# Kernel optimization log

Measured on AMD Instinct MI355X. Metric: run time of the kernel, lower is better.

The kernel has to match this reference:

```python
import jax, jax.numpy as jnp
import numpy as np

VOCAB, EMB, H1, H2, T, B = 21, 128, 64, 100, 500, 1024


def lstm(x, W_ih, W_hh, b_ih, b_hh):
    # x: [B, T, D]; torch gate order i, f, g, o
    Bx, H = x.shape[0], W_hh.shape[1]
    xproj = jnp.einsum('btd,gd->btg', x, W_ih) + b_ih  # [B, T, 4H]

    def step(carry, xt):
        h, c = carry
        gates = xt + h @ W_hh.T + b_hh
        i, f, g, o = jnp.split(gates, 4, axis=-1)
        c = jax.nn.sigmoid(f) * c + jax.nn.sigmoid(i) * jnp.tanh(g)
        h = jax.nn.sigmoid(o) * jnp.tanh(c)
        return (h, c), h

    h0 = jnp.zeros((Bx, H), x.dtype)
    _, hs = jax.lax.scan(step, (h0, h0), xproj.transpose(1, 0, 2))
    return hs.transpose(1, 0, 2)  # [B, T, H]


def setup_inputs() -> dict:
    key = jax.random.key(0)
    ks = jax.random.split(key, 12)
    s = 0.05
    x_idx = jax.random.randint(ks[0], (B, T), 0, VOCAB, dtype=jnp.int32)
    emb_table = jax.random.normal(ks[1], (VOCAB, EMB), jnp.float32) * s
    emb_table = emb_table.at[0].set(0.0)  # padding_idx=0
    d = dict(
        x_idx=x_idx,
        emb_table=emb_table,
        W_ih1=jax.random.normal(ks[2], (4 * H1, EMB), jnp.float32) * s,
        W_hh1=jax.random.normal(ks[3], (4 * H1, H1), jnp.float32) * s,
        b_ih1=jax.random.normal(ks[4], (4 * H1,), jnp.float32) * s,
        b_hh1=jax.random.normal(ks[5], (4 * H1,), jnp.float32) * s,
        W_ih2=jax.random.normal(ks[6], (4 * H2, H1), jnp.float32) * s,
        W_hh2=jax.random.normal(ks[7], (4 * H2, H2), jnp.float32) * s,
        b_ih2=jax.random.normal(ks[8], (4 * H2,), jnp.float32) * s,
        b_hh2=jax.random.normal(ks[9], (4 * H2,), jnp.float32) * s,
        fc_w=jax.random.normal(ks[10], (1, H2), jnp.float32) * s,
        fc_b=jax.random.normal(ks[11], (1,), jnp.float32) * s,
    )
    return d


def reference(x_idx, emb_table, W_ih1, W_hh1, b_ih1, b_hh1,
              W_ih2, W_hh2, b_ih2, b_hh2, fc_w, fc_b):
    # embedding with padding_idx=0 (row is zero; mask keeps grads faithful)
    x = emb_table[x_idx] * (x_idx != 0)[..., None].astype(emb_table.dtype)  # [B,T,128]
    x = lstm(x, W_ih1, W_hh1, b_ih1, b_hh1)  # [B,T,64]
    # MaxPool1d(kernel=5, stride=5) over time
    Bx, Tx, D = x.shape
    Tp = Tx // 5
    x = x[:, :Tp * 5].reshape(Bx, Tp, 5, D).max(axis=2)  # [B,T/5,64]
    x = lstm(x, W_ih2, W_hh2, b_ih2, b_hh2)  # [B,T/5,100]
    h = x[:, -1, :]
    return jax.nn.sigmoid(h @ fc_w.T + fc_b)  # [B,1]
```

## Files before the change

kernel.cpp:

```cpp
#include <hip/hip_runtime.h>

#define VOCAB 21
#define EMB 128
#define H1 64
#define H2 100
#define T1 500
#define TP 100
#define NB 1024
#define LOG2E 1.44269504f

typedef __attribute__((ext_vector_type(8))) short bf16x8;
typedef __attribute__((ext_vector_type(4))) float f32x4;

__device__ __forceinline__ unsigned short f2bf(float x){
    union { float f; unsigned u; } v; v.f = x;
    return (unsigned short)((v.u + 0x8000u) >> 16);
}
__device__ __forceinline__ void bar_lds(){
    asm volatile("s_waitcnt lgkmcnt(0)\n\ts_barrier" ::: "memory");
}
__device__ __forceinline__ void wait_lds(){
    asm volatile("s_waitcnt lgkmcnt(0)" ::: "memory");
}
__device__ __forceinline__ float ex2(float x){ return __builtin_amdgcn_exp2f(x); }
__device__ __forceinline__ float rcp(float x){ return __builtin_amdgcn_rcpf(x); }

__global__ void k_table(const float* __restrict__ Wih, const float* __restrict__ emb,
                        const float* __restrict__ bih, const float* __restrict__ bhh,
                        float* __restrict__ table){
    const int p = threadIdx.x;
    const int v = blockIdx.x;
    const int orig = (p & 3) * H1 + (p >> 2);
    float s = bih[orig] + bhh[orig];
    if (v != 0){
        const float* w = Wih + orig * EMB;
        const float* e = emb + v * EMB;
        #pragma unroll 16
        for (int d = 0; d < EMB; ++d) s += w[d]*e[d];
    }
    table[v*256 + p] = s * LOG2E;
}

__global__ __launch_bounds__(256, 1) void k_lstm1(
    const int* __restrict__ xidx, const float* __restrict__ Whh,
    const float* __restrict__ tbl_g, float* __restrict__ x2){
  __shared__ __align__(16) float table[VOCAB*256];
  __shared__ __align__(16) unsigned short hbuf[2][16*64];
  __shared__ __align__(16) f32x4 glds[4*16*4];
  __shared__ int idxs[4*T1];

  const int tid = threadIdx.x;
  const int w = tid >> 6, l = tid & 63;
  const int b0 = blockIdx.x * 4;
  const int n = l & 15, kg = l >> 4;

  for (int i = tid; i < VOCAB*256; i += 256) table[i] = tbl_g[i];
  for (int i = tid; i < 4*T1; i += 256){
      int r = i / T1, t = i - r*T1;
      idxs[i] = xidx[(b0 + r)*T1 + t];
  }
  { unsigned short* hz = (unsigned short*)hbuf;
    for (int i = tid; i < 2048; i += 256) hz[i] = 0; }

  bf16x8 af[4][2];
  #pragma unroll
  for (int u = 0; u < 4; ++u){
      const int p = 16*(4*w + u) + n;
      const int orig = (p & 3)*H1 + (p >> 2);
      #pragma unroll
      for (int c = 0; c < 2; ++c){
          const float* src = Whh + orig*H1 + c*32 + kg*8;
          bf16x8 f;
          #pragma unroll
          for (int j = 0; j < 8; ++j) f[j] = (short)f2bf(src[j] * LOG2E);
          af[u][c] = f;
      }
  }

  char* hb = (char*)hbuf;
  char* gb = (char*)glds + 1024*w;
  const int swz = (n & 7) << 4;
  const int rb0 = (n*128 + 16*kg) ^ swz;
  const int rb1 = (n*128 + 64 + 16*kg) ^ swz;
  const int cell = 16*w + (l >> 2);
  const int r_c  = l & 3;
  const int wbh  = (r_c*128 + 2*cell) ^ (r_c << 4);
  const float twoL = 2.0f * LOG2E;

  float cc = 0.f, pm = -1e30f;
  __syncthreads();

  int vnext = idxs[r_c*T1];
  f32x4 tvq = *(const f32x4*)&table[vnext*256 + 4*cell];
  vnext = idxs[r_c*T1 + 1];
  const f32x4 z4 = {0.f, 0.f, 0.f, 0.f};

  int rp = 0, tm = 0, tp = 0;
  for (int t = 0; t < T1; ++t){
      bf16x8 bf0 = *(const bf16x8*)(hb + rp + rb0);
      bf16x8 bf1 = *(const bf16x8*)(hb + rp + rb1);
      #pragma unroll
      for (int u = 0; u < 4; ++u){
          f32x4 a = __builtin_amdgcn_mfma_f32_16x16x32_bf16(af[u][0], bf0, z4, 0,0,0);
          a        = __builtin_amdgcn_mfma_f32_16x16x32_bf16(af[u][1], bf1, a, 0,0,0);
          if (n < 4)
              *(f32x4*)(gb + 256*u + 64*kg + 16*n) = a;
      }
      wait_lds();
      f32x4 q = *(const f32x4*)(gb + 16*l);
      f32x4 tvn = *(const f32x4*)&table[vnext*256 + 4*cell];
      int vn2 = idxs[r_c*T1 + ((t + 2 < T1) ? (t + 2) : 0)];
      float gi = q[0] + tvq[0];
      float gf = q[1] + tvq[1];
      float gg = q[2] + tvq[2];
      float go = q[3] + tvq[3];
      float si = rcp(1.f + ex2(-gi));
      float sf = rcp(1.f + ex2(-gf));
      float so = rcp(1.f + ex2(-go));
      float tg = 1.f - 2.f*rcp(1.f + ex2(gg + gg));
      cc = sf*cc + si*tg;
      float th = 1.f - 2.f*rcp(1.f + ex2(twoL*cc));
      float h = so*th;
      const int wp = rp ^ 2048;
      *(unsigned short*)(hb + wp + wbh) = f2bf(h);
      pm = fmaxf(pm, h);
      if (++tm == 5){
          x2[(b0 + r_c)*(TP*H1) + tp*H1 + cell] = pm;
          pm = -1e30f; tm = 0; ++tp;
      }
      tvq = tvn; vnext = vn2;
      rp = wp;
      bar_lds();
  }
}

__global__ __launch_bounds__(512, 1) void k_lstm2(
    const float* __restrict__ x2, const float* __restrict__ Wih,
    const float* __restrict__ Whh, const float* __restrict__ bih,
    const float* __restrict__ bhh, const float* __restrict__ fcw,
    const float* __restrict__ fcb, float* __restrict__ out){
  __shared__ __align__(16) unsigned short blds[2][16*192];
  __shared__ __align__(16) f32x4 gl2[108*4];
  __shared__ float fcred[8][4];

  const int tid = threadIdx.x;
  const int w = tid >> 6, l = tid & 63;
  const int b0 = blockIdx.x * 4;
  const int n = l & 15, kg = l >> 4;
  const int tlo = (w < 2) ? 4*w : 8 + 3*(w - 2);
  const int nt  = (w < 2) ? 4 : 3;

  { unsigned* bz0 = (unsigned*)blds;
    for (int i = tid; i < 3072; i += 512) bz0[i] = 0; }
  { float* gz = (float*)gl2;
    for (int i = tid; i < 432*4; i += 512) gz[i] = 0.f; }

  bf16x8 af[4][6];
  #pragma unroll
  for (int u = 0; u < 4; ++u){
      if (u < nt){
          const int p = 16*(tlo + u) + n;
          const int cell_ = p >> 2, gate = p & 3;
          #pragma unroll
          for (int c = 0; c < 6; ++c){
              bf16x8 f;
              #pragma unroll
              for (int jj = 0; jj < 8; ++jj){
                  int k = c*32 + kg*8 + jj;
                  float vv = 0.f;
                  if (cell_ < H2){
                      if (k < 64)           vv = Wih[(gate*H2 + cell_)*H1 + k];
                      else if (k < 64 + H2) vv = Whh[(gate*H2 + cell_)*H2 + (k - 64)];
                  }
                  f[jj] = (short)f2bf(vv * LOG2E);
              }
              af[u][c] = f;
          }
      }
  }

  f32x4 bz[4];
  #pragma unroll
  for (int u = 0; u < 4; ++u){
      const int cu = 4*(tlo + u) + kg;
      f32x4 b = {0.f,0.f,0.f,0.f};
      if (u < nt && cu < H2){
          #pragma unroll
          for (int g = 0; g < 4; ++g) b[g] = (bih[g*H2 + cu] + bhh[g*H2 + cu]) * LOG2E;
      }
      bz[u] = b;
  }

  const bool act = (l >> 2) < 4*nt;
  const int cellc = 4*tlo + (l >> 2);
  const int r_c = l & 3;
  const float fwv = (act && cellc < H2) ? fcw[cellc] : 0.f;
  const float twoL = 2.0f * LOG2E;

  char* bb = (char*)blds;
  char* gb = (char*)gl2;
  const int swz = (n & 7) << 4;
  int rb[6];
  #pragma unroll
  for (int c = 0; c < 6; ++c) rb[c] = (n*384 + 64*c + 16*kg) ^ swz;
  const int wbh = (r_c*384 + 2*(64 + cellc)) ^ (r_c << 4);

  const int xr = (tid >> 5) & 3, xc = tid & 31;
  const int xwb = (xr*384 + 4*xc) ^ (xr << 4);
  if (tid >= 384){
      float2 v = *(const float2*)&x2[(b0 + xr)*(TP*H1) + 2*xc];
      unsigned pk = (unsigned)f2bf(v.x) | ((unsigned)f2bf(v.y) << 16);
      *(unsigned*)(bb + xwb) = pk;
  }
  float cc = 0.f, hv = 0.f;
  __syncthreads();

  int rp = 0;
  for (int t = 0; t < TP; ++t){
      float2 xn = {0.f, 0.f};
      if (tid >= 384 && t + 1 < TP)
          xn = *(const float2*)&x2[(b0 + xr)*(TP*H1) + (t+1)*H1 + 2*xc];
      bf16x8 bf[6];
      #pragma unroll
      for (int c = 0; c < 6; ++c) bf[c] = *(const bf16x8*)(bb + rp + rb[c]);
      #pragma unroll
      for (int u = 0; u < 4; ++u){
          if (u < nt){
              f32x4 za = __builtin_amdgcn_mfma_f32_16x16x32_bf16(af[u][0], bf[0], bz[u], 0,0,0);
              f32x4 zb = __builtin_amdgcn_mfma_f32_16x16x32_bf16(af[u][1], bf[1], (f32x4){0.f,0.f,0.f,0.f}, 0,0,0);
              za = __builtin_amdgcn_mfma_f32_16x16x32_bf16(af[u][2], bf[2], za, 0,0,0);
              zb = __builtin_amdgcn_mfma_f32_16x16x32_bf16(af[u][3], bf[3], zb, 0,0,0);
              za = __builtin_amdgcn_mfma_f32_16x16x32_bf16(af[u][4], bf[4], za, 0,0,0);
              zb = __builtin_amdgcn_mfma_f32_16x16x32_bf16(af[u][5], bf[5], zb, 0,0,0);
              f32x4 z = za + zb;
              if (n < 4)
                  *(f32x4*)(gb + 256*(tlo + u) + 64*kg + 16*n) = z;
          }
      }
      wait_lds();
      const int wp = rp ^ 6144;
      if (act){
          f32x4 q = *(const f32x4*)(gb + 256*tlo + 16*l);
          float si = rcp(1.f + ex2(-q[0]));
          float sf = rcp(1.f + ex2(-q[1]));
          float so = rcp(1.f + ex2(-q[3]));
          float tg = 1.f - 2.f*rcp(1.f + ex2(q[2] + q[2]));
          cc = sf*cc + si*tg;
          float th = 1.f - 2.f*rcp(1.f + ex2(twoL*cc));
          hv = so*th;
          *(unsigned short*)(bb + wp + wbh) = f2bf(hv);
      }
      if (tid >= 384 && t + 1 < TP){
          unsigned pk = (unsigned)f2bf(xn.x) | ((unsigned)f2bf(xn.y) << 16);
          *(unsigned*)(bb + wp + xwb) = pk;
      }
      rp = wp;
      bar_lds();
  }

  float p = (act && cellc < H2) ? hv * fwv : 0.f;
  p += __shfl_xor(p, 4);
  p += __shfl_xor(p, 8);
  p += __shfl_xor(p, 16);
  p += __shfl_xor(p, 32);
  if (l < 4) fcred[w][l] = p;
  __syncthreads();
  if (tid < 4){
      float s = 0.f;
      #pragma unroll
      for (int ww = 0; ww < 8; ++ww) s += fcred[ww][tid];
      s += fcb[0];
      out[b0 + tid] = rcp(1.f + ex2(-s * LOG2E));
  }
}

extern "C" void kernel_launch(void* const* d_in, const int* in_sizes, int n_in,
                              void* d_out, int out_size, void* d_ws, size_t ws_size,
                              hipStream_t stream) {
    const int*   x_idx = (const int*)  d_in[0];
    const float* emb   = (const float*)d_in[1];
    const float* Wih1  = (const float*)d_in[2];
    const float* Whh1  = (const float*)d_in[3];
    const float* bih1  = (const float*)d_in[4];
    const float* bhh1  = (const float*)d_in[5];
    const float* Wih2  = (const float*)d_in[6];
    const float* Whh2  = (const float*)d_in[7];
    const float* bih2  = (const float*)d_in[8];
    const float* bhh2  = (const float*)d_in[9];
    const float* fcw   = (const float*)d_in[10];
    const float* fcb   = (const float*)d_in[11];
    float* out = (float*)d_out;

    float* table = (float*)d_ws;
    float* x2    = (float*)((char*)d_ws + 32768);

    k_table<<<VOCAB, 256, 0, stream>>>(Wih1, emb, bih1, bhh1, table);
    k_lstm1<<<NB / 4, 256, 0, stream>>>(x_idx, Whh1, table, x2);
    k_lstm2<<<NB / 4, 512, 0, stream>>>(x2, Wih2, Whh2, bih2, bhh2, fcw, fcb, out);
}
```

Before: 319.5 us.

## Compute LSTM cell updates directly from MFMA accumulators, removing the LDS gate exchange

Both LSTM kernels stop writing MFMA gate results to shared memory and reading them back through a wait. Instead, lanes that already hold the four gate values of a cell (n<4) apply the activations in registers and write h straight into the bf16 hidden buffer. Layer 1 adds the embedding-projection table term as the MFMA accumulator input and pads the table row stride to 260 to spread LDS banks. Layer 2 prefetches x two steps ahead. The cost is that only a quarter of the lanes do the transcendental work, each handling four cells serially, which lengthens that part of every step.

```diff
diff --git a/kernel.cpp b/kernel.cpp
--- a/kernel.cpp
+++ b/kernel.cpp
@@ -7,6 +7,7 @@
 #define T1 500
 #define TP 100
 #define NB 1024
+#define TBL_LD 260
 #define LOG2E 1.44269504f
 
 typedef __attribute__((ext_vector_type(8))) short bf16x8;
@@ -18,9 +19,6 @@
 }
 __device__ __forceinline__ void bar_lds(){
     asm volatile("s_waitcnt lgkmcnt(0)\n\ts_barrier" ::: "memory");
-}
-__device__ __forceinline__ void wait_lds(){
-    asm volatile("s_waitcnt lgkmcnt(0)" ::: "memory");
 }
 __device__ __forceinline__ float ex2(float x){ return __builtin_amdgcn_exp2f(x); }
 __device__ __forceinline__ float rcp(float x){ return __builtin_amdgcn_rcpf(x); }
@@ -38,15 +36,14 @@
         #pragma unroll 16
         for (int d = 0; d < EMB; ++d) s += w[d]*e[d];
     }
-    table[v*256 + p] = s * LOG2E;
+    table[v*TBL_LD + p] = s * LOG2E;
 }
 
 __global__ __launch_bounds__(256, 1) void k_lstm1(
     const int* __restrict__ xidx, const float* __restrict__ Whh,
     const float* __restrict__ tbl_g, float* __restrict__ x2){
-  __shared__ __align__(16) float table[VOCAB*256];
+  __shared__ __align__(16) float table[VOCAB*TBL_LD];
   __shared__ __align__(16) unsigned short hbuf[2][16*64];
-  __shared__ __align__(16) f32x4 glds[4*16*4];
   __shared__ int idxs[4*T1];
 
   const int tid = threadIdx.x;
@@ -54,7 +51,7 @@
   const int b0 = blockIdx.x * 4;
   const int n = l & 15, kg = l >> 4;
 
-  for (int i = tid; i < VOCAB*256; i += 256) table[i] = tbl_g[i];
+  for (int i = tid; i < VOCAB*TBL_LD; i += 256) table[i] = tbl_g[i];
   for (int i = tid; i < 4*T1; i += 256){
       int r = i / T1, t = i - r*T1;
       idxs[i] = xidx[(b0 + r)*T1 + t];
@@ -78,57 +75,73 @@
   }
 
   char* hb = (char*)hbuf;
-  char* gb = (char*)glds + 1024*w;
   const int swz = (n & 7) << 4;
   const int rb0 = (n*128 + 16*kg) ^ swz;
   const int rb1 = (n*128 + 64 + 16*kg) ^ swz;
-  const int cell = 16*w + (l >> 2);
-  const int r_c  = l & 3;
-  const int wbh  = (r_c*128 + 2*cell) ^ (r_c << 4);
+  const bool prod = (n < 4);
+  const int rowc = n & 3;
+  int cu[4], whb[4];
+  #pragma unroll
+  for (int u = 0; u < 4; ++u){
+      cu[u] = 16*w + 4*u + kg;
+      whb[u] = (n*128 + 2*cu[u]) ^ swz;
+  }
   const float twoL = 2.0f * LOG2E;
 
-  float cc = 0.f, pm = -1e30f;
+  float cc[4] = {0.f,0.f,0.f,0.f};
+  float pm[4] = {-1e30f,-1e30f,-1e30f,-1e30f};
   __syncthreads();
 
-  int vnext = idxs[r_c*T1];
-  f32x4 tvq = *(const f32x4*)&table[vnext*256 + 4*cell];
-  vnext = idxs[r_c*T1 + 1];
+  int vv = idxs[rowc*T1];
+  f32x4 tq[4];
+  #pragma unroll
+  for (int u = 0; u < 4; ++u) tq[u] = *(const f32x4*)&table[vv*TBL_LD + 4*cu[u]];
+  int vnext = idxs[rowc*T1 + 1];
   const f32x4 z4 = {0.f, 0.f, 0.f, 0.f};
 
   int rp = 0, tm = 0, tp = 0;
   for (int t = 0; t < T1; ++t){
       bf16x8 bf0 = *(const bf16x8*)(hb + rp + rb0);
       bf16x8 bf1 = *(const bf16x8*)(hb + rp + rb1);
+      f32x4 tqn[4];
+      #pragma unroll
+      for (int u = 0; u < 4; ++u)
+          tqn[u] = *(const f32x4*)&table[vnext*TBL_LD + 4*cu[u]];
+      int vn2 = idxs[rowc*T1 + ((t + 2 < T1) ? (t + 2) : 0)];
+      f32x4 z[4];
       #pragma unroll
       for (int u = 0; u < 4; ++u){
-          f32x4 a = __builtin_amdgcn_mfma_f32_16x16x32_bf16(af[u][0], bf0, z4, 0,0,0);
-          a        = __builtin_amdgcn_mfma_f32_16x16x32_bf16(af[u][1], bf1, a, 0,0,0);
-          if (n < 4)
-              *(f32x4*)(gb + 256*u + 64*kg + 16*n) = a;
-      }
-      wait_lds();
-      f32x4 q = *(const f32x4*)(gb + 16*l);
-      f32x4 tvn = *(const f32x4*)&table[vnext*256 + 4*cell];
-      int vn2 = idxs[r_c*T1 + ((t + 2 < T1) ? (t + 2) : 0)];
-      float gi = q[0] + tvq[0];
-      float gf = q[1] + tvq[1];
-      float gg = q[2] + tvq[2];
-      float go = q[3] + tvq[3];
-      float si = rcp(1.f + ex2(-gi));
-      float sf = rcp(1.f + ex2(-gf));
-      float so = rcp(1.f + ex2(-go));
-      float tg = 1.f - 2.f*rcp(1.f + ex2(gg + gg));
-      cc = sf*cc + si*tg;
-      float th = 1.f - 2.f*rcp(1.f + ex2(twoL*cc));
-      float h = so*th;
+          f32x4 a = __builtin_amdgcn_mfma_f32_16x16x32_bf16(af[u][0], bf0, tq[u], 0,0,0);
+          f32x4 b = __builtin_amdgcn_mfma_f32_16x16x32_bf16(af[u][1], bf1, z4, 0,0,0);
+          z[u] = a + b;
+      }
       const int wp = rp ^ 2048;
-      *(unsigned short*)(hb + wp + wbh) = f2bf(h);
-      pm = fmaxf(pm, h);
-      if (++tm == 5){
-          x2[(b0 + r_c)*(TP*H1) + tp*H1 + cell] = pm;
-          pm = -1e30f; tm = 0; ++tp;
-      }
-      tvq = tvn; vnext = vn2;
+      ++tm;
+      if (prod){
+          #pragma unroll
+          for (int u = 0; u < 4; ++u){
+              float si = rcp(1.f + ex2(-z[u][0]));
+              float sf = rcp(1.f + ex2(-z[u][1]));
+              float so = rcp(1.f + ex2(-z[u][3]));
+              float tg = 1.f - 2.f*rcp(1.f + ex2(z[u][2] + z[u][2]));
+              cc[u] = sf*cc[u] + si*tg;
+              float th = 1.f - 2.f*rcp(1.f + ex2(twoL*cc[u]));
+              float h = so*th;
+              *(unsigned short*)(hb + wp + whb[u]) = f2bf(h);
+              pm[u] = fmaxf(pm[u], h);
+          }
+          if (tm == 5){
+              float* dst = x2 + (b0 + n)*(TP*H1) + tp*H1;
+              #pragma unroll
+              for (int u = 0; u < 4; ++u) dst[cu[u]] = pm[u];
+              #pragma unroll
+              for (int u = 0; u < 4; ++u) pm[u] = -1e30f;
+          }
+      }
+      if (tm == 5){ tm = 0; ++tp; }
+      #pragma unroll
+      for (int u = 0; u < 4; ++u) tq[u] = tqn[u];
+      vnext = vn2;
       rp = wp;
       bar_lds();
   }
@@ -140,7 +153,6 @@
     const float* __restrict__ bhh, const float* __restrict__ fcw,
     const float* __restrict__ fcb, float* __restrict__ out){
   __shared__ __align__(16) unsigned short blds[2][16*192];
-  __shared__ __align__(16) f32x4 gl2[108*4];
   __shared__ float fcred[8][4];
 
   const int tid = threadIdx.x;
@@ -152,8 +164,6 @@
 
   { unsigned* bz0 = (unsigned*)blds;
     for (int i = tid; i < 3072; i += 512) bz0[i] = 0; }
-  { float* gz = (float*)gl2;
-    for (int i = tid; i < 432*4; i += 512) gz[i] = 0.f; }
 
   bf16x8 af[4][6];
   #pragma unroll
@@ -180,49 +190,52 @@
   }
 
   f32x4 bz[4];
+  int cu[4], whb[4];
+  float fw[4];
   #pragma unroll
   for (int u = 0; u < 4; ++u){
-      const int cu = 4*(tlo + u) + kg;
+      cu[u] = 4*(tlo + u) + kg;
       f32x4 b = {0.f,0.f,0.f,0.f};
-      if (u < nt && cu < H2){
-          #pragma unroll
-          for (int g = 0; g < 4; ++g) b[g] = (bih[g*H2 + cu] + bhh[g*H2 + cu]) * LOG2E;
-      }
-      bz[u] = b;
-  }
-
-  const bool act = (l >> 2) < 4*nt;
-  const int cellc = 4*tlo + (l >> 2);
-  const int r_c = l & 3;
-  const float fwv = (act && cellc < H2) ? fcw[cellc] : 0.f;
+      float fv = 0.f;
+      if (u < nt && cu[u] < H2){
+          #pragma unroll
+          for (int g = 0; g < 4; ++g) b[g] = (bih[g*H2 + cu[u]] + bhh[g*H2 + cu[u]]) * LOG2E;
+          fv = fcw[cu[u]];
+      }
+      bz[u] = b; fw[u] = fv;
+      whb[u] = (n*384 + 2*(64 + cu[u])) ^ ((n & 7) << 4);
+  }
+  const bool prod = (n < 4);
   const float twoL = 2.0f * LOG2E;
 
   char* bb = (char*)blds;
-  char* gb = (char*)gl2;
   const int swz = (n & 7) << 4;
   int rb[6];
   #pragma unroll
   for (int c = 0; c < 6; ++c) rb[c] = (n*384 + 64*c + 16*kg) ^ swz;
-  const int wbh = (r_c*384 + 2*(64 + cellc)) ^ (r_c << 4);
 
   const int xr = (tid >> 5) & 3, xc = tid & 31;
   const int xwb = (xr*384 + 4*xc) ^ (xr << 4);
+  float2 xa = {0.f, 0.f};
   if (tid >= 384){
       float2 v = *(const float2*)&x2[(b0 + xr)*(TP*H1) + 2*xc];
       unsigned pk = (unsigned)f2bf(v.x) | ((unsigned)f2bf(v.y) << 16);
       *(unsigned*)(bb + xwb) = pk;
-  }
-  float cc = 0.f, hv = 0.f;
+      xa = *(const float2*)&x2[(b0 + xr)*(TP*H1) + 1*H1 + 2*xc];
+  }
+  float cc[4] = {0.f,0.f,0.f,0.f};
+  float hv[4] = {0.f,0.f,0.f,0.f};
   __syncthreads();
 
   int rp = 0;
   for (int t = 0; t < TP; ++t){
-      float2 xn = {0.f, 0.f};
-      if (tid >= 384 && t + 1 < TP)
-          xn = *(const float2*)&x2[(b0 + xr)*(TP*H1) + (t+1)*H1 + 2*xc];
+      float2 xb_ = {0.f, 0.f};
+      if (tid >= 384 && t + 2 < TP)
+          xb_ = *(const float2*)&x2[(b0 + xr)*(TP*H1) + (t+2)*H1 + 2*xc];
       bf16x8 bf[6];
       #pragma unroll
       for (int c = 0; c < 6; ++c) bf[c] = *(const bf16x8*)(bb + rp + rb[c]);
+      f32x4 z[4];
       #pragma unroll
       for (int u = 0; u < 4; ++u){
           if (u < nt){
@@ -232,35 +245,41 @@
               zb = __builtin_amdgcn_mfma_f32_16x16x32_bf16(af[u][3], bf[3], zb, 0,0,0);
               za = __builtin_amdgcn_mfma_f32_16x16x32_bf16(af[u][4], bf[4], za, 0,0,0);
               zb = __builtin_amdgcn_mfma_f32_16x16x32_bf16(af[u][5], bf[5], zb, 0,0,0);
-              f32x4 z = za + zb;
-              if (n < 4)
-                  *(f32x4*)(gb + 256*(tlo + u) + 64*kg + 16*n) = z;
-          }
-      }
-      wait_lds();
+              z[u] = za + zb;
+          }
+      }
       const int wp = rp ^ 6144;
-      if (act){
-          f32x4 q = *(const f32x4*)(gb + 256*tlo + 16*l);
-          float si = rcp(1.f + ex2(-q[0]));
-          float sf = rcp(1.f + ex2(-q[1]));
-          float so = rcp(1.f + ex2(-q[3]));
-          float tg = 1.f - 2.f*rcp(1.f + ex2(q[2] + q[2]));
-          cc = sf*cc + si*tg;
-          float th = 1.f - 2.f*rcp(1.f + ex2(twoL*cc));
-          hv = so*th;
-          *(unsigned short*)(bb + wp + wbh) = f2bf(hv);
+      if (prod){
+          #pragma unroll
+          for (int u = 0; u < 4; ++u){
+              if (u < nt){
+                  float si = rcp(1.f + ex2(-z[u][0]));
+                  float sf = rcp(1.f + ex2(-z[u][1]));
+                  float so = rcp(1.f + ex2(-z[u][3]));
+                  float tg = 1.f - 2.f*rcp(1.f + ex2(z[u][2] + z[u][2]));
+                  cc[u] = sf*cc[u] + si*tg;
+                  float th = 1.f - 2.f*rcp(1.f + ex2(twoL*cc[u]));
+                  hv[u] = so*th;
+                  if (cu[u] < H2)
+                      *(unsigned short*)(bb + wp + whb[u]) = f2bf(hv[u]);
+              }
+          }
       }
       if (tid >= 384 && t + 1 < TP){
-          unsigned pk = (unsigned)f2bf(xn.x) | ((unsigned)f2bf(xn.y) << 16);
+          unsigned pk = (unsigned)f2bf(xa.x) | ((unsigned)f2bf(xa.y) << 16);
           *(unsigned*)(bb + wp + xwb) = pk;
       }
+      xa = xb_;
       rp = wp;
       bar_lds();
   }
 
-  float p = (act && cellc < H2) ? hv * fwv : 0.f;
-  p += __shfl_xor(p, 4);
-  p += __shfl_xor(p, 8);
+  float p = 0.f;
+  if (prod){
+      #pragma unroll
+      for (int u = 0; u < 4; ++u)
+          if (u < nt && cu[u] < H2) p += hv[u] * fw[u];
+  }
   p += __shfl_xor(p, 16);
   p += __shfl_xor(p, 32);
   if (l < 4) fcred[w][l] = p;
```

New measurement: 441.4 us. +38.2%, slower.

## Halve batch per block to double grid size and split MFMA accumulation chains

Applied to the files above, without the earlier changes.

Each block of both LSTM kernels now handles 2 sequences instead of 4, doubling the grid to 512 blocks so more CUs are busy on MI355X's 256-CU device and raising launch-bound occupancy hints. The dependent MFMA pair in layer 1 is split into two independent accumulations summed afterwards, which shortens the per-step serial latency. The embedding table row stride is padded to 260 floats to reduce LDS bank conflicts, and layer-2 input prefetch is restructured to load one float per thread two steps ahead. Half the MFMA columns now go unused, so total MFMA work per batch element doubles.

```diff
diff --git a/kernel.cpp b/kernel.cpp
--- a/kernel.cpp
+++ b/kernel.cpp
@@ -7,6 +7,7 @@
 #define T1 500
 #define TP 100
 #define NB 1024
+#define TBL_LD 260
 #define LOG2E 1.44269504f
 
 typedef __attribute__((ext_vector_type(8))) short bf16x8;
@@ -38,29 +39,31 @@
         #pragma unroll 16
         for (int d = 0; d < EMB; ++d) s += w[d]*e[d];
     }
-    table[v*256 + p] = s * LOG2E;
-}
-
-__global__ __launch_bounds__(256, 1) void k_lstm1(
+    table[v*TBL_LD + p] = s * LOG2E;
+}
+
+__global__ __launch_bounds__(256, 2) void k_lstm1(
     const int* __restrict__ xidx, const float* __restrict__ Whh,
     const float* __restrict__ tbl_g, float* __restrict__ x2){
-  __shared__ __align__(16) float table[VOCAB*256];
+  __shared__ __align__(16) float table[VOCAB*TBL_LD];
   __shared__ __align__(16) unsigned short hbuf[2][16*64];
-  __shared__ __align__(16) f32x4 glds[4*16*4];
-  __shared__ int idxs[4*T1];
+  __shared__ __align__(16) f32x4 glds[4][64];
+  __shared__ int idxs[2*T1];
 
   const int tid = threadIdx.x;
   const int w = tid >> 6, l = tid & 63;
-  const int b0 = blockIdx.x * 4;
+  const int b0 = blockIdx.x * 2;
   const int n = l & 15, kg = l >> 4;
 
-  for (int i = tid; i < VOCAB*256; i += 256) table[i] = tbl_g[i];
-  for (int i = tid; i < 4*T1; i += 256){
+  for (int i = tid; i < VOCAB*TBL_LD; i += 256) table[i] = tbl_g[i];
+  for (int i = tid; i < 2*T1; i += 256){
       int r = i / T1, t = i - r*T1;
       idxs[i] = xidx[(b0 + r)*T1 + t];
   }
   { unsigned short* hz = (unsigned short*)hbuf;
     for (int i = tid; i < 2048; i += 256) hz[i] = 0; }
+  { float* gz = (float*)glds;
+    for (int i = tid; i < 1024; i += 256) gz[i] = 0.f; }
 
   bf16x8 af[4][2];
   #pragma unroll
@@ -84,15 +87,17 @@
   const int rb1 = (n*128 + 64 + 16*kg) ^ swz;
   const int cell = 16*w + (l >> 2);
   const int r_c  = l & 3;
-  const int wbh  = (r_c*128 + 2*cell) ^ (r_c << 4);
+  const bool act = r_c < 2;
+  const int rv = l & 1;
+  const int wbh = (r_c*128 + 2*cell) ^ (r_c << 4);
   const float twoL = 2.0f * LOG2E;
 
   float cc = 0.f, pm = -1e30f;
   __syncthreads();
 
-  int vnext = idxs[r_c*T1];
-  f32x4 tvq = *(const f32x4*)&table[vnext*256 + 4*cell];
-  vnext = idxs[r_c*T1 + 1];
+  int vv = idxs[rv*T1];
+  f32x4 tq = *(const f32x4*)&table[vv*TBL_LD + 4*cell];
+  int vnext = idxs[rv*T1 + 1];
   const f32x4 z4 = {0.f, 0.f, 0.f, 0.f};
 
   int rp = 0, tm = 0, tp = 0;
@@ -102,18 +107,19 @@
       #pragma unroll
       for (int u = 0; u < 4; ++u){
           f32x4 a = __builtin_amdgcn_mfma_f32_16x16x32_bf16(af[u][0], bf0, z4, 0,0,0);
-          a        = __builtin_amdgcn_mfma_f32_16x16x32_bf16(af[u][1], bf1, a, 0,0,0);
-          if (n < 4)
-              *(f32x4*)(gb + 256*u + 64*kg + 16*n) = a;
+          f32x4 b = __builtin_amdgcn_mfma_f32_16x16x32_bf16(af[u][1], bf1, z4, 0,0,0);
+          f32x4 z = a + b;
+          if (n < 2)
+              *(f32x4*)(gb + 256*u + 64*kg + 16*n) = z;
       }
       wait_lds();
       f32x4 q = *(const f32x4*)(gb + 16*l);
-      f32x4 tvn = *(const f32x4*)&table[vnext*256 + 4*cell];
-      int vn2 = idxs[r_c*T1 + ((t + 2 < T1) ? (t + 2) : 0)];
-      float gi = q[0] + tvq[0];
-      float gf = q[1] + tvq[1];
-      float gg = q[2] + tvq[2];
-      float go = q[3] + tvq[3];
+      f32x4 tvn = *(const f32x4*)&table[vnext*TBL_LD + 4*cell];
+      int vn2 = idxs[rv*T1 + ((t + 2 < T1) ? (t + 2) : 0)];
+      float gi = q[0] + tq[0];
+      float gf = q[1] + tq[1];
+      float gg = q[2] + tq[2];
+      float go = q[3] + tq[3];
       float si = rcp(1.f + ex2(-gi));
       float sf = rcp(1.f + ex2(-gf));
       float so = rcp(1.f + ex2(-go));
@@ -122,30 +128,31 @@
       float th = 1.f - 2.f*rcp(1.f + ex2(twoL*cc));
       float h = so*th;
       const int wp = rp ^ 2048;
-      *(unsigned short*)(hb + wp + wbh) = f2bf(h);
+      if (act) *(unsigned short*)(hb + wp + wbh) = f2bf(h);
       pm = fmaxf(pm, h);
       if (++tm == 5){
-          x2[(b0 + r_c)*(TP*H1) + tp*H1 + cell] = pm;
+          if (act)
+              x2[(b0 + r_c)*(TP*H1) + tp*H1 + cell] = pm;
           pm = -1e30f; tm = 0; ++tp;
       }
-      tvq = tvn; vnext = vn2;
+      tq = tvn; vnext = vn2;
       rp = wp;
       bar_lds();
   }
 }
 
-__global__ __launch_bounds__(512, 1) void k_lstm2(
+__global__ __launch_bounds__(512, 4) void k_lstm2(
     const float* __restrict__ x2, const float* __restrict__ Wih,
     const float* __restrict__ Whh, const float* __restrict__ bih,
     const float* __restrict__ bhh, const float* __restrict__ fcw,
     const float* __restrict__ fcb, float* __restrict__ out){
   __shared__ __align__(16) unsigned short blds[2][16*192];
   __shared__ __align__(16) f32x4 gl2[108*4];
-  __shared__ float fcred[8][4];
+  __shared__ float fcred[8][2];
 
   const int tid = threadIdx.x;
   const int w = tid >> 6, l = tid & 63;
-  const int b0 = blockIdx.x * 4;
+  const int b0 = blockIdx.x * 2;
   const int n = l & 15, kg = l >> 4;
   const int tlo = (w < 2) ? 4*w : 8 + 3*(w - 2);
   const int nt  = (w < 2) ? 4 : 3;
@@ -194,6 +201,7 @@
   const bool act = (l >> 2) < 4*nt;
   const int cellc = 4*tlo + (l >> 2);
   const int r_c = l & 3;
+  const bool actr = act && (r_c < 2) && (cellc < H2);
   const float fwv = (act && cellc < H2) ? fcw[cellc] : 0.f;
   const float twoL = 2.0f * LOG2E;
 
@@ -205,21 +213,23 @@
   for (int c = 0; c < 6; ++c) rb[c] = (n*384 + 64*c + 16*kg) ^ swz;
   const int wbh = (r_c*384 + 2*(64 + cellc)) ^ (r_c << 4);
 
-  const int xr = (tid >> 5) & 3, xc = tid & 31;
-  const int xwb = (xr*384 + 4*xc) ^ (xr << 4);
+  const int xi = tid - 384;
+  const int xr = xi >> 6, xcell = xi & 63;
+  const int xwb = (xr*384 + 2*xcell) ^ (xr << 4);
+  float xa = 0.f;
   if (tid >= 384){
-      float2 v = *(const float2*)&x2[(b0 + xr)*(TP*H1) + 2*xc];
-      unsigned pk = (unsigned)f2bf(v.x) | ((unsigned)f2bf(v.y) << 16);
-      *(unsigned*)(bb + xwb) = pk;
+      float v = x2[(b0 + xr)*(TP*H1) + xcell];
+      *(unsigned short*)(bb + xwb) = f2bf(v);
+      xa = x2[(b0 + xr)*(TP*H1) + 1*H1 + xcell];
   }
   float cc = 0.f, hv = 0.f;
   __syncthreads();
 
   int rp = 0;
   for (int t = 0; t < TP; ++t){
-      float2 xn = {0.f, 0.f};
-      if (tid >= 384 && t + 1 < TP)
-          xn = *(const float2*)&x2[(b0 + xr)*(TP*H1) + (t+1)*H1 + 2*xc];
+      float xb_ = 0.f;
+      if (tid >= 384 && t + 2 < TP)
+          xb_ = x2[(b0 + xr)*(TP*H1) + (t+2)*H1 + xcell];
       bf16x8 bf[6];
       #pragma unroll
       for (int c = 0; c < 6; ++c) bf[c] = *(const bf16x8*)(bb + rp + rb[c]);
@@ -233,39 +243,36 @@
               za = __builtin_amdgcn_mfma_f32_16x16x32_bf16(af[u][4], bf[4], za, 0,0,0);
               zb = __builtin_amdgcn_mfma_f32_16x16x32_bf16(af[u][5], bf[5], zb, 0,0,0);
               f32x4 z = za + zb;
-              if (n < 4)
+              if (n < 2)
                   *(f32x4*)(gb + 256*(tlo + u) + 64*kg + 16*n) = z;
           }
       }
       wait_lds();
+      f32x4 q = *(const f32x4*)(gb + 256*tlo + 16*l);
+      float si = rcp(1.f + ex2(-q[0]));
+      float sf = rcp(1.f + ex2(-q[1]));
+      float so = rcp(1.f + ex2(-q[3]));
+      float tg = 1.f - 2.f*rcp(1.f + ex2(q[2] + q[2]));
+      cc = sf*cc + si*tg;
+      float th = 1.f - 2.f*rcp(1.f + ex2(twoL*cc));
+      hv = so*th;
       const int wp = rp ^ 6144;
-      if (act){
-          f32x4 q = *(const f32x4*)(gb + 256*tlo + 16*l);
-          float si = rcp(1.f + ex2(-q[0]));
-          float sf = rcp(1.f + ex2(-q[1]));
-          float so = rcp(1.f + ex2(-q[3]));
-          float tg = 1.f - 2.f*rcp(1.f + ex2(q[2] + q[2]));
-          cc = sf*cc + si*tg;
-          float th = 1.f - 2.f*rcp(1.f + ex2(twoL*cc));
-          hv = so*th;
-          *(unsigned short*)(bb + wp + wbh) = f2bf(hv);
-      }
-      if (tid >= 384 && t + 1 < TP){
-          unsigned pk = (unsigned)f2bf(xn.x) | ((unsigned)f2bf(xn.y) << 16);
-          *(unsigned*)(bb + wp + xwb) = pk;
-      }
+      if (actr) *(unsigned short*)(bb + wp + wbh) = f2bf(hv);
+      if (tid >= 384 && t + 1 < TP)
+          *(unsigned short*)(bb + wp + xwb) = f2bf(xa);
+      xa = xb_;
       rp = wp;
       bar_lds();
   }
 
-  float p = (act && cellc < H2) ? hv * fwv : 0.f;
+  float p = actr ? hv * fwv : 0.f;
   p += __shfl_xor(p, 4);
   p += __shfl_xor(p, 8);
   p += __shfl_xor(p, 16);
   p += __shfl_xor(p, 32);
-  if (l < 4) fcred[w][l] = p;
+  if (l < 2) fcred[w][l] = p;
   __syncthreads();
-  if (tid < 4){
+  if (tid < 2){
       float s = 0.f;
       #pragma unroll
       for (int ww = 0; ww < 8; ++ww) s += fcred[ww][tid];
@@ -295,6 +302,6 @@
     float* x2    = (float*)((char*)d_ws + 32768);
 
     k_table<<<VOCAB, 256, 0, stream>>>(Wih1, emb, bih1, bhh1, table);
-    k_lstm1<<<NB / 4, 256, 0, stream>>>(x_idx, Whh1, table, x2);
-    k_lstm2<<<NB / 4, 512, 0, stream>>>(x2, Wih2, Whh2, bih2, bhh2, fcw, fcb, out);
-}
+    k_lstm1<<<NB / 2, 256, 0, stream>>>(x_idx, Whh1, table, x2);
+    k_lstm2<<<NB / 2, 512, 0, stream>>>(x2, Wih2, Whh2, bih2, bhh2, fcw, fcb, out);
+}
```

New measurement: 542.7 us. 69.9% more time.

## Restructure LSTM1 to 16 batches per block with one MFMA tile per wave

Applied to the files above, without the earlier changes.

Layer-1 LSTM blocks now handle 16 batch rows with 1024 threads instead of 4 rows with 256 threads. Each wave owns one 16-gate tile, and its MFMA output lanes map directly to the four gates of a cell, so the LDS round trip for gate redistribution goes away. The input-projection table entry is passed as the MFMA accumulator, which removes the separate adds, and the table row stride is padded to 260 to avoid bank conflicts. Grid size drops from 256 to 64 blocks, so fewer CUs are busy, and each step has a 1024-thread barrier. All 16 rows are now used in the MFMA N dimension where only 4 were useful before.

```diff
diff --git a/kernel.cpp b/kernel.cpp
--- a/kernel.cpp
+++ b/kernel.cpp
@@ -7,6 +7,7 @@
 #define T1 500
 #define TP 100
 #define NB 1024
+#define TBL_LD 260
 #define LOG2E 1.44269504f
 
 typedef __attribute__((ext_vector_type(8))) short bf16x8;
@@ -38,86 +39,71 @@
         #pragma unroll 16
         for (int d = 0; d < EMB; ++d) s += w[d]*e[d];
     }
-    table[v*256 + p] = s * LOG2E;
-}
-
-__global__ __launch_bounds__(256, 1) void k_lstm1(
+    table[v*TBL_LD + p] = s * LOG2E;
+}
+
+__global__ __launch_bounds__(1024, 1) void k_lstm1(
     const int* __restrict__ xidx, const float* __restrict__ Whh,
     const float* __restrict__ tbl_g, float* __restrict__ x2){
-  __shared__ __align__(16) float table[VOCAB*256];
+  __shared__ __align__(16) float table[VOCAB*TBL_LD];
   __shared__ __align__(16) unsigned short hbuf[2][16*64];
-  __shared__ __align__(16) f32x4 glds[4*16*4];
-  __shared__ int idxs[4*T1];
+  __shared__ int idxs[16*T1];
 
   const int tid = threadIdx.x;
-  const int w = tid >> 6, l = tid & 63;
-  const int b0 = blockIdx.x * 4;
-  const int n = l & 15, kg = l >> 4;
-
-  for (int i = tid; i < VOCAB*256; i += 256) table[i] = tbl_g[i];
-  for (int i = tid; i < 4*T1; i += 256){
+  const int gt = tid >> 6, l = tid & 63;
+  const int b0 = blockIdx.x * 16;
+  const int row = l & 15, kg = l >> 4;
+
+  for (int i = tid; i < VOCAB*TBL_LD; i += 1024) table[i] = tbl_g[i];
+  for (int i = tid; i < 16*T1; i += 1024){
       int r = i / T1, t = i - r*T1;
       idxs[i] = xidx[(b0 + r)*T1 + t];
   }
   { unsigned short* hz = (unsigned short*)hbuf;
-    for (int i = tid; i < 2048; i += 256) hz[i] = 0; }
-
-  bf16x8 af[4][2];
-  #pragma unroll
-  for (int u = 0; u < 4; ++u){
-      const int p = 16*(4*w + u) + n;
+    for (int i = tid; i < 2048; i += 1024) hz[i] = 0; }
+
+  bf16x8 af0, af1;
+  {
+      const int p = 16*gt + row;
       const int orig = (p & 3)*H1 + (p >> 2);
-      #pragma unroll
-      for (int c = 0; c < 2; ++c){
-          const float* src = Whh + orig*H1 + c*32 + kg*8;
-          bf16x8 f;
-          #pragma unroll
-          for (int j = 0; j < 8; ++j) f[j] = (short)f2bf(src[j] * LOG2E);
-          af[u][c] = f;
-      }
+      bf16x8 f;
+      const float* s0 = Whh + orig*H1 + kg*8;
+      #pragma unroll
+      for (int j = 0; j < 8; ++j) f[j] = (short)f2bf(s0[j] * LOG2E);
+      af0 = f;
+      const float* s1 = Whh + orig*H1 + 32 + kg*8;
+      #pragma unroll
+      for (int j = 0; j < 8; ++j) f[j] = (short)f2bf(s1[j] * LOG2E);
+      af1 = f;
   }
 
   char* hb = (char*)hbuf;
-  char* gb = (char*)glds + 1024*w;
-  const int swz = (n & 7) << 4;
-  const int rb0 = (n*128 + 16*kg) ^ swz;
-  const int rb1 = (n*128 + 64 + 16*kg) ^ swz;
-  const int cell = 16*w + (l >> 2);
-  const int r_c  = l & 3;
-  const int wbh  = (r_c*128 + 2*cell) ^ (r_c << 4);
+  const int swz = (row & 7) << 4;
+  const int rb0 = (row*128 + 16*kg) ^ swz;
+  const int rb1 = (row*128 + 64 + 16*kg) ^ swz;
+  const int cell = 4*gt + kg;
+  const int wbh  = (row*128 + 2*cell) ^ swz;
   const float twoL = 2.0f * LOG2E;
 
   float cc = 0.f, pm = -1e30f;
   __syncthreads();
 
-  int vnext = idxs[r_c*T1];
-  f32x4 tvq = *(const f32x4*)&table[vnext*256 + 4*cell];
-  vnext = idxs[r_c*T1 + 1];
-  const f32x4 z4 = {0.f, 0.f, 0.f, 0.f};
+  int vv = idxs[row*T1];
+  f32x4 tq = *(const f32x4*)&table[vv*TBL_LD + 4*cell];
+  int vnext = idxs[row*T1 + 1];
 
   int rp = 0, tm = 0, tp = 0;
   for (int t = 0; t < T1; ++t){
       bf16x8 bf0 = *(const bf16x8*)(hb + rp + rb0);
       bf16x8 bf1 = *(const bf16x8*)(hb + rp + rb1);
-      #pragma unroll
-      for (int u = 0; u < 4; ++u){
-          f32x4 a = __builtin_amdgcn_mfma_f32_16x16x32_bf16(af[u][0], bf0, z4, 0,0,0);
-          a        = __builtin_amdgcn_mfma_f32_16x16x32_bf16(af[u][1], bf1, a, 0,0,0);
-          if (n < 4)
-              *(f32x4*)(gb + 256*u + 64*kg + 16*n) = a;
-      }
-      wait_lds();
-      f32x4 q = *(const f32x4*)(gb + 16*l);
-      f32x4 tvn = *(const f32x4*)&table[vnext*256 + 4*cell];
-      int vn2 = idxs[r_c*T1 + ((t + 2 < T1) ? (t + 2) : 0)];
-      float gi = q[0] + tvq[0];
-      float gf = q[1] + tvq[1];
-      float gg = q[2] + tvq[2];
-      float go = q[3] + tvq[3];
-      float si = rcp(1.f + ex2(-gi));
-      float sf = rcp(1.f + ex2(-gf));
-      float so = rcp(1.f + ex2(-go));
-      float tg = 1.f - 2.f*rcp(1.f + ex2(gg + gg));
+      f32x4 a = __builtin_amdgcn_mfma_f32_16x16x32_bf16(af0, bf0, tq, 0,0,0);
+      f32x4 z = __builtin_amdgcn_mfma_f32_16x16x32_bf16(af1, bf1, a, 0,0,0);
+      f32x4 tqn = *(const f32x4*)&table[vnext*TBL_LD + 4*cell];
+      int vn2 = idxs[row*T1 + ((t + 2 < T1) ? (t + 2) : 0)];
+      float si = rcp(1.f + ex2(-z[0]));
+      float sf = rcp(1.f + ex2(-z[1]));
+      float so = rcp(1.f + ex2(-z[3]));
+      float tg = 1.f - 2.f*rcp(1.f + ex2(z[2] + z[2]));
       cc = sf*cc + si*tg;
       float th = 1.f - 2.f*rcp(1.f + ex2(twoL*cc));
       float h = so*th;
@@ -125,10 +111,10 @@
       *(unsigned short*)(hb + wp + wbh) = f2bf(h);
       pm = fmaxf(pm, h);
       if (++tm == 5){
-          x2[(b0 + r_c)*(TP*H1) + tp*H1 + cell] = pm;
+          x2[(b0 + row)*(TP*H1) + tp*H1 + cell] = pm;
           pm = -1e30f; tm = 0; ++tp;
       }
-      tvq = tvn; vnext = vn2;
+      tq = tqn; vnext = vn2;
       rp = wp;
       bar_lds();
   }
@@ -295,6 +281,6 @@
     float* x2    = (float*)((char*)d_ws + 32768);
 
     k_table<<<VOCAB, 256, 0, stream>>>(Wih1, emb, bih1, bhh1, table);
-    k_lstm1<<<NB / 4, 256, 0, stream>>>(x_idx, Whh1, table, x2);
+    k_lstm1<<<NB / 16, 1024, 0, stream>>>(x_idx, Whh1, table, x2);
     k_lstm2<<<NB / 4, 512, 0, stream>>>(x2, Wih2, Whh2, bih2, bhh2, fcw, fcb, out);
 }
```

Measured after the change: 320.8 us. No clear change (+0.4%).
